# Performance work log

Hardware: AMD Instinct MI355X
Metric: run time of the kernel (lower is better)

## Reference

```python
import jax, jax.numpy as jnp
import numpy as np

HID = 2048   # hidden_size
H = 16       # num_attention_heads
KV = 2       # num_key_value_heads
HD = 256     # head_dim
S = 2048     # seq_len (prefill)
MAX_SEQ = 4096
EPS = 1e-6
RD = HD // 4          # partial RoPE dims (head_dim * 0.25)
SCALE = HD ** (-0.5)
GROUPS = H // KV


def setup_inputs() -> dict:
    key = jax.random.key(0)
    ks = jax.random.split(key, 10)
    hidden_in = jax.random.normal(ks[0], (1, S, HID), jnp.float32)
    ang = jax.random.uniform(ks[1], (1, S, RD), jnp.float32) * (2.0 * np.pi)
    cos = jnp.cos(ang)
    sin = jnp.sin(ang)
    w = 0.02
    q_proj_w = jax.random.normal(ks[2], (2 * H * HD, HID), jnp.float32) * w
    k_proj_w = jax.random.normal(ks[3], (KV * HD, HID), jnp.float32) * w
    v_proj_w = jax.random.normal(ks[4], (KV * HD, HID), jnp.float32) * w
    o_proj_w = jax.random.normal(ks[5], (HID, H * HD), jnp.float32) * w
    q_norm_w = jax.random.normal(ks[6], (HD,), jnp.float32) * 0.1
    k_norm_w = jax.random.normal(ks[7], (HD,), jnp.float32) * 0.1
    return dict(hidden_in=hidden_in, cos=cos, sin=sin,
                q_proj_w=q_proj_w, k_proj_w=k_proj_w, v_proj_w=v_proj_w,
                o_proj_w=o_proj_w, q_norm_w=q_norm_w, k_norm_w=k_norm_w)


def _rmsnorm(x, w):
    var = jnp.mean(x * x, axis=-1, keepdims=True)
    return x * jax.lax.rsqrt(var + EPS) * (1.0 + w)


def _rotate_half(x):
    x1, x2 = jnp.split(x, 2, axis=-1)
    return jnp.concatenate([-x2, x1], axis=-1)


def reference(hidden_in, cos, sin, q_proj_w, k_proj_w, v_proj_w, o_proj_w, q_norm_w, k_norm_w):
    # projections (F.linear => x @ W^T)
    qg = hidden_in @ q_proj_w.T                      # [1, S, 2*H*HD]
    k = hidden_in @ k_proj_w.T                       # [1, S, KV*HD]
    v = hidden_in @ v_proj_w.T

    qg = qg.reshape(1, S, H, 2 * HD)
    q, gate = qg[..., :HD], qg[..., HD:]             # chunk(2, dim=-1)
    gate = gate.reshape(1, S, H * HD)

    q = _rmsnorm(q, q_norm_w).transpose(0, 2, 1, 3)  # [1, H, S, HD]
    k = _rmsnorm(k.reshape(1, S, KV, HD), k_norm_w).transpose(0, 2, 1, 3)  # [1, KV, S, HD]
    v = v.reshape(1, S, KV, HD).transpose(0, 2, 1, 3)                      # [1, KV, S, HD]

    # partial RoPE on first RD dims
    c = cos[:, None, :, :]                           # [1, 1, S, RD]
    s = sin[:, None, :, :]
    q_rot, q_pass = q[..., :RD], q[..., RD:]
    k_rot, k_pass = k[..., :RD], k[..., RD:]
    q = jnp.concatenate([q_rot * c + _rotate_half(q_rot) * s, q_pass], axis=-1)
    k = jnp.concatenate([k_rot * c + _rotate_half(k_rot) * s, k_pass], axis=-1)

    # KV cache padded to max_seq
    zpad = jnp.zeros((1, KV, MAX_SEQ - S, HD), k.dtype)
    k_cache_out = jnp.concatenate([k, zpad], axis=2)
    v_cache_out = jnp.concatenate([v, zpad], axis=2)

    # GQA repeat
    k_r = jnp.repeat(k, GROUPS, axis=1)              # [1, H, S, HD]
    v_r = jnp.repeat(v, GROUPS, axis=1)

    causal = jnp.triu(jnp.full((S, S), -10000.0, jnp.float32), k=1)
    scores = jnp.einsum('bhqd,bhkd->bhqk', q, k_r) * SCALE + causal
    attn_w = jax.nn.softmax(scores, axis=-1)
    attn = jnp.einsum('bhqk,bhkd->bhqd', attn_w, v_r)
    attn = attn.transpose(0, 2, 1, 3).reshape(1, S, H * HD)

    attn = attn * jax.nn.sigmoid(gate)
    hidden_out = attn @ o_proj_w.T                   # [1, S, HID]
    return hidden_out, k_cache_out, v_cache_out
```

## Files before the change

### kernel.cpp

```cpp
#include <hip/hip_runtime.h>

#define S_LEN 2048
#define HID 2048
#define NH 16
#define NKV 2
#define HD 256
#define MAXSEQ 4096
#define NALL 9216
#define RD 64

typedef __attribute__((ext_vector_type(8))) short short8_t;
typedef __attribute__((ext_vector_type(4))) float float4_t;

#define DPPF(x, ctrl) __builtin_bit_cast(float, __builtin_amdgcn_update_dpp( \
    __builtin_bit_cast(int, x), __builtin_bit_cast(int, x), ctrl, 0xF, 0xF, false))

__device__ __forceinline__ unsigned short f2b(float f) {
  union { float f; unsigned u; } v; v.f = f;
  unsigned u = v.u;
  return (unsigned short)((u + 0x7FFFu + ((u >> 16) & 1u)) >> 16);
}

__device__ __forceinline__ void gload_lds16(const void* g, void* l) {
  __builtin_amdgcn_global_load_lds(
      (const __attribute__((address_space(1))) void*)g,
      (__attribute__((address_space(3))) void*)l, 16, 0, 0);
}

__global__ void fused_cvt(const float* __restrict__ hidden, const float* __restrict__ qw,
                          const float* __restrict__ kw, const float* __restrict__ vw,
                          const float* __restrict__ ow,
                          unsigned short* __restrict__ hidb, unsigned short* __restrict__ wallb,
                          unsigned short* __restrict__ wob,
                          float* __restrict__ kcache, float* __restrict__ vcache) {
  const long i = (long)blockIdx.x * 256 + threadIdx.x;
  const long N0 = 1048576, N1 = N0 + 4194304, N2 = N1 + 262144, N3 = N2 + 262144,
             N4 = N3 + 2097152;
  if (i < N4) {
    const float* s; unsigned short* d; long j;
    if (i < N0)      { s = hidden; d = hidb;  j = i; }
    else if (i < N1) { s = qw; d = wallb;                        j = i - N0; }
    else if (i < N2) { s = kw; d = wallb + (size_t)8192*HID;     j = i - N1; }
    else if (i < N3) { s = vw; d = wallb + (size_t)8704*HID;     j = i - N2; }
    else             { s = ow; d = wob;                          j = i - N3; }
    float4 v = ((const float4*)s)[j];
    short4 o;
    o.x = (short)f2b(v.x); o.y = (short)f2b(v.y);
    o.z = (short)f2b(v.z); o.w = (short)f2b(v.w);
    ((short4*)d)[j] = o;
  } else {
    long j = i - N4;
    int region = (int)(j >> 17);
    long o = j & 131071;
    float* base = (region < 2 ? kcache : vcache)
                + (size_t)(region & 1) * MAXSEQ * HD + (size_t)S_LEN * HD;
    float4 z; z.x = 0.f; z.y = 0.f; z.z = 0.f; z.w = 0.f;
    ((float4*)base)[o] = z;
  }
}

template<int BM, int BN, int MI, int NI>
__global__ __launch_bounds__(256, 2) void gemm_bt(
    const unsigned short* __restrict__ A, const unsigned short* __restrict__ B,
    float* __restrict__ C, int M, int N, int K) {
  constexpr int BK = 64;
  __shared__ unsigned short As[BM * BK];
  __shared__ unsigned short Bs[BN * BK];
  const int tid = threadIdx.x;
  const int lane = tid & 63;
  const int w = tid >> 6;
  const int wr = w >> 1, wc = w & 1;
  const int l15 = lane & 15, l4 = lane >> 4;
  const int M0 = blockIdx.y * BM, N0 = blockIdx.x * BN;
  float4_t acc[MI][NI] = {};
  for (int kt = 0; kt < K; kt += BK) {
    __syncthreads();
#pragma unroll
    for (int i = 0; i < BM/32; ++i) {
      int c = tid + i*256;
      int row = c >> 3;
      gload_lds16(A + (size_t)(M0 + row)*K + kt + ((c & 7) ^ (row & 7))*8, (char*)As + c*16);
    }
#pragma unroll
    for (int i = 0; i < BN/32; ++i) {
      int c = tid + i*256;
      int row = c >> 3;
      gload_lds16(B + (size_t)(N0 + row)*K + kt + ((c & 7) ^ (row & 7))*8, (char*)Bs + c*16);
    }
    __syncthreads();
#pragma unroll
    for (int ks = 0; ks < 2; ++ks) {
      short8_t af[MI], bf[NI];
#pragma unroll
      for (int mi = 0; mi < MI; ++mi) {
        int row = wr*(BM/2) + mi*16 + l15;
        af[mi] = *(const short8_t*)&As[row*BK + ((ks*4 + l4) ^ (l15 & 7))*8];
      }
#pragma unroll
      for (int ni = 0; ni < NI; ++ni) {
        int row = wc*(BN/2) + ni*16 + l15;
        bf[ni] = *(const short8_t*)&Bs[row*BK + ((ks*4 + l4) ^ (l15 & 7))*8];
      }
#pragma unroll
      for (int mi = 0; mi < MI; ++mi)
#pragma unroll
        for (int ni = 0; ni < NI; ++ni)
          acc[mi][ni] = __builtin_amdgcn_mfma_f32_16x16x32_bf16(af[mi], bf[ni], acc[mi][ni], 0, 0, 0);
    }
  }
#pragma unroll
  for (int mi = 0; mi < MI; ++mi) {
    int rb = M0 + wr*(BM/2) + mi*16 + l4*4;
#pragma unroll
    for (int ni = 0; ni < NI; ++ni) {
      int col = N0 + wc*(BN/2) + ni*16 + l15;
#pragma unroll
      for (int r = 0; r < 4; ++r)
        C[(size_t)(rb + r)*N + col] = acc[mi][ni][r];
    }
  }
}

__global__ void postproc(const float* __restrict__ C1,
                         const float* __restrict__ cosb, const float* __restrict__ sinb,
                         const float* __restrict__ qnw, const float* __restrict__ knw,
                         unsigned short* __restrict__ qb, unsigned short* __restrict__ kb,
                         unsigned short* __restrict__ vtb,
                         float* __restrict__ kcache, float* __restrict__ vcache) {
  const int w = threadIdx.x >> 6, lane = threadIdx.x & 63;
  const int s = blockIdx.x*4 + w;
  const int t = blockIdx.y;
  const int d = lane*4;
  const float* rowp;
  if (t < 16)      rowp = C1 + (size_t)s*NALL + t*512;
  else if (t < 18) rowp = C1 + (size_t)s*NALL + 8192 + (t-16)*256;
  else             rowp = C1 + (size_t)s*NALL + 8704 + (t-18)*256;
  float4 x = *(const float4*)(rowp + d);
  if (t >= 18) {
    int kvi = t - 18;
    *(float4*)(vcache + (size_t)kvi*MAXSEQ*HD + (size_t)s*HD + d) = x;
    unsigned short* vt = vtb + (size_t)kvi*HD*S_LEN;
    vt[(size_t)(d+0)*S_LEN + s] = f2b(x.x);
    vt[(size_t)(d+1)*S_LEN + s] = f2b(x.y);
    vt[(size_t)(d+2)*S_LEN + s] = f2b(x.z);
    vt[(size_t)(d+3)*S_LEN + s] = f2b(x.w);
    return;
  }
  float ss = x.x*x.x + x.y*x.y + x.z*x.z + x.w*x.w;
#pragma unroll
  for (int o = 32; o >= 1; o >>= 1) ss += __shfl_xor(ss, o, 64);
  float rn = rsqrtf(ss*(1.0f/256.0f) + 1e-6f);
  const float* nw = (t < 16) ? qnw : knw;
  float4 g = *(const float4*)(nw + d);
  float4 y;
  y.x = x.x*rn*(1.f+g.x); y.y = x.y*rn*(1.f+g.y);
  y.z = x.z*rn*(1.f+g.z); y.w = x.w*rn*(1.f+g.w);
  float px = __shfl_xor(y.x, 8, 64);
  float py = __shfl_xor(y.y, 8, 64);
  float pz = __shfl_xor(y.z, 8, 64);
  float pw = __shfl_xor(y.w, 8, 64);
  if (lane < 16) {
    float sgn = (lane & 8) ? 1.f : -1.f;
    float4 cs = *(const float4*)(cosb + (size_t)s*RD + d);
    float4 sn = *(const float4*)(sinb + (size_t)s*RD + d);
    y.x = y.x*cs.x + sgn*px*sn.x;
    y.y = y.y*cs.y + sgn*py*sn.y;
    y.z = y.z*cs.z + sgn*pz*sn.z;
    y.w = y.w*cs.w + sgn*pw*sn.w;
  }
  if (t < 16) {
    const float qs = 0.0625f * 1.44269504088896f;
    short4 o;
    o.x = (short)f2b(y.x*qs); o.y = (short)f2b(y.y*qs);
    o.z = (short)f2b(y.z*qs); o.w = (short)f2b(y.w*qs);
    *(short4*)(qb + (size_t)t*S_LEN*HD + (size_t)s*HD + d) = o;
  } else {
    int kvi = t - 16;
    *(float4*)(kcache + (size_t)kvi*MAXSEQ*HD + (size_t)s*HD + d) = y;
    short4 o;
    o.x = (short)f2b(y.x); o.y = (short)f2b(y.y);
    o.z = (short)f2b(y.z); o.w = (short)f2b(y.w);
    *(short4*)(kb + (size_t)kvi*S_LEN*HD + (size_t)s*HD + d) = o;
  }
}

__global__ __launch_bounds__(512, 2) void attn_kernel(
    const unsigned short* __restrict__ qb, const unsigned short* __restrict__ kb,
    const unsigned short* __restrict__ vtb, const float* __restrict__ C1,
    unsigned short* __restrict__ attnb) {
  __shared__ char smem[139264];
  const int tid = threadIdx.x, lane = tid & 63, w = tid >> 6;
  const int g  = w >> 2;
  const int wq = w & 3;
  const int l15 = lane & 15, l4 = lane >> 4;
  unsigned short* Pw = (unsigned short*)(smem + 131072 + w*1024);
  const int b = blockIdx.x;
  const int h = b & 15;
  const int pi = b >> 4;
  const int kv = h >> 3;
  const unsigned short* Qb = qb + (size_t)h*S_LEN*HD;
  const unsigned short* Kb = kb + (size_t)kv*S_LEN*HD;
  const unsigned short* Vb = vtb + (size_t)kv*HD*S_LEN;

  auto STAGE = [&](int k0s, int buf) {
    char* KsD = smem + buf*32768;
    char* VTD = smem + 65536 + buf*32768;
#pragma unroll
    for (int i = 0; i < 4; ++i) {
      int c = tid + i*512;
      int row = c >> 5;
      gload_lds16(Kb + (size_t)(k0s + row)*HD + ((c & 31) ^ (row & 7))*8, KsD + c*16);
    }
#pragma unroll
    for (int i = 0; i < 4; ++i) {
      int c = tid + i*512;
      int row = c >> 3;
      gload_lds16(Vb + (size_t)row*S_LEN + k0s + ((c & 7) ^ (row & 7))*8, VTD + c*16);
    }
  };

  for (int ph = 0; ph < 2; ++ph) {
    const int qt = ph ? (31 - pi) : pi;
    const int q0 = qt * 64;
    const int qrow = q0 + wq*16 + l15;
    short8_t qf[8];
#pragma unroll
    for (int kk = 0; kk < 8; ++kk)
      qf[kk] = *(const short8_t*)(Qb + (size_t)qrow*HD + kk*32 + l4*8);
    float4_t oacc[16] = {};
    float m_run[4] = {-1e29f, -1e29f, -1e29f, -1e29f};
    float l_run[4] = {0.f, 0.f, 0.f, 0.f};
    const int nT = qt + 1;
    __syncthreads();
    STAGE(0, 0);
    for (int t = 0; t < nT; ++t) {
      const int cur = t & 1;
      const int k0 = t * 64;
      if (t + 1 < nT) {
        STAGE((t + 1) * 64, cur ^ 1);
        asm volatile("s_waitcnt vmcnt(8)" ::: "memory");
      } else {
        asm volatile("s_waitcnt vmcnt(0)" ::: "memory");
      }
      __builtin_amdgcn_s_barrier();
      __builtin_amdgcn_sched_barrier(0);
      const unsigned short* Ks  = (const unsigned short*)(smem + cur*32768);
      const unsigned short* VTs = (const unsigned short*)(smem + 65536 + cur*32768);
      float4_t sacc[2] = {};
#pragma unroll
      for (int nt = 0; nt < 2; ++nt)
#pragma unroll
        for (int kk = 0; kk < 8; ++kk) {
          int krow = g*32 + nt*16 + l15;
          short8_t bfr = *(const short8_t*)&Ks[krow*HD + ((kk*4 + l4) ^ (l15 & 7))*8];
          sacc[nt] = __builtin_amdgcn_mfma_f32_16x16x32_bf16(qf[kk], bfr, sacc[nt], 0, 0, 0);
        }
      if (t == qt) {
#pragma unroll
        for (int nt = 0; nt < 2; ++nt)
#pragma unroll
          for (int r = 0; r < 4; ++r)
            if (k0 + g*32 + nt*16 + l15 > q0 + wq*16 + l4*4 + r) sacc[nt][r] = -1e30f;
      }
      float m0[4], p[2][4];
#pragma unroll
      for (int r = 0; r < 4; ++r) {
        float v = fmaxf(sacc[0][r], sacc[1][r]);
        v = fmaxf(v, DPPF(v, 0xB1));
        v = fmaxf(v, DPPF(v, 0x4E));
        v = fmaxf(v, DPPF(v, 0x141));
        v = fmaxf(v, DPPF(v, 0x140));
        m0[r] = v;
      }
      int need = (m0[0] > m_run[0] + 4.f) | (m0[1] > m_run[1] + 4.f) |
                 (m0[2] > m_run[2] + 4.f) | (m0[3] > m_run[3] + 4.f);
      if (__any(need)) {
        float al[4];
#pragma unroll
        for (int r = 0; r < 4; ++r) {
          float mnew = fmaxf(m_run[r], m0[r]);
          al[r] = exp2f(m_run[r] - mnew);
          m_run[r] = mnew;
          l_run[r] *= al[r];
        }
#pragma unroll
        for (int nt2 = 0; nt2 < 16; ++nt2) {
          oacc[nt2][0] *= al[0];
          oacc[nt2][1] *= al[1];
          oacc[nt2][2] *= al[2];
          oacc[nt2][3] *= al[3];
        }
      }
#pragma unroll
      for (int r = 0; r < 4; ++r) {
        p[0][r] = exp2f(sacc[0][r] - m_run[r]);
        p[1][r] = exp2f(sacc[1][r] - m_run[r]);
        float sum = p[0][r] + p[1][r];
        sum += DPPF(sum, 0xB1);
        sum += DPPF(sum, 0x4E);
        sum += DPPF(sum, 0x141);
        sum += DPPF(sum, 0x140);
        l_run[r] += sum;
      }
#pragma unroll
      for (int nt = 0; nt < 2; ++nt)
#pragma unroll
        for (int r = 0; r < 4; ++r) {
          int prow = l4*4 + r;
          int pcol = nt*16 + l15;
          Pw[prow*32 + (((pcol >> 3) ^ ((prow >> 1) & 3)))*8 + (pcol & 7)] = f2b(p[nt][r]);
        }
      short8_t pf = *(const short8_t*)&Pw[l15*32 + ((l4 ^ ((l15 >> 1) & 3)))*8];
#pragma unroll
      for (int nt2 = 0; nt2 < 16; ++nt2) {
        int vrow = nt2*16 + l15;
        short8_t v0 = *(const short8_t*)&VTs[vrow*64 + ((4*g + l4) ^ (vrow & 7))*8];
        oacc[nt2] = __builtin_amdgcn_mfma_f32_16x16x32_bf16(pf, v0, oacc[nt2], 0, 0, 0);
      }
      asm volatile("" ::: "memory");
      __builtin_amdgcn_s_barrier();
    }
    __syncthreads();
    float* Od = (float*)smem;
    float* ML = (float*)(smem + 69632);
    const int r0 = wq*16 + l4*4;
    if (g == 1) {
#pragma unroll
      for (int r = 0; r < 4; ++r)
        if (l15 == 0) { ML[(r0 + r)*2] = m_run[r]; ML[(r0 + r)*2 + 1] = l_run[r]; }
#pragma unroll
      for (int nt2 = 0; nt2 < 16; ++nt2) {
        int dim = nt2*16 + l15;
#pragma unroll
        for (int r = 0; r < 4; ++r)
          Od[(r0 + r)*258 + dim] = oacc[nt2][r];
      }
    }
    __syncthreads();
    if (g == 0) {
      float fA[4], fB[4], inv_l[4];
#pragma unroll
      for (int r = 0; r < 4; ++r) {
        float mB = ML[(r0 + r)*2];
        float lB = ML[(r0 + r)*2 + 1];
        float m = fmaxf(m_run[r], mB);
        fA[r] = exp2f(m_run[r] - m);
        fB[r] = exp2f(mB - m);
        inv_l[r] = 1.f / (l_run[r]*fA[r] + lB*fB[r]);
      }
      const int srow0 = q0 + r0;
#pragma unroll
      for (int nt2 = 0; nt2 < 16; ++nt2) {
        int dim = nt2*16 + l15;
#pragma unroll
        for (int r = 0; r < 4; ++r) {
          int srow = srow0 + r;
          float ov = oacc[nt2][r]*fA[r] + Od[(r0 + r)*258 + dim]*fB[r];
          float gv = C1[(size_t)srow*NALL + h*512 + 256 + dim];
          float sg = 1.f / (1.f + __expf(-gv));
          attnb[(size_t)srow*(NH*HD) + h*HD + dim] = f2b(ov * inv_l[r] * sg);
        }
      }
    }
  }
}

extern "C" void kernel_launch(void* const* d_in, const int* in_sizes, int n_in,
                              void* d_out, int out_size, void* d_ws, size_t ws_size,
                              hipStream_t stream) {
  const float* hidden = (const float*)d_in[0];
  const float* cosb   = (const float*)d_in[1];
  const float* sinb   = (const float*)d_in[2];
  const float* qw     = (const float*)d_in[3];
  const float* kw     = (const float*)d_in[4];
  const float* vw     = (const float*)d_in[5];
  const float* ow     = (const float*)d_in[6];
  const float* qnw    = (const float*)d_in[7];
  const float* knw    = (const float*)d_in[8];
  float* out    = (float*)d_out;
  float* kcache = out + (size_t)S_LEN*HID;
  float* vcache = kcache + (size_t)NKV*MAXSEQ*HD;

  char* ws = (char*)d_ws;
  size_t off = 0;
  auto alloc = [&](size_t bytes) -> char* {
    char* p = ws + off; off += (bytes + 255) & ~(size_t)255; return p;
  };
  unsigned short* hidb  = (unsigned short*)alloc((size_t)S_LEN*HID*2);
  unsigned short* wallb = (unsigned short*)alloc((size_t)NALL*HID*2);
  unsigned short* wob   = (unsigned short*)alloc((size_t)HID*NH*HD*2);
  float*          C1    = (float*)alloc((size_t)S_LEN*NALL*4);
  unsigned short* qb    = (unsigned short*)alloc((size_t)NH*S_LEN*HD*2);
  unsigned short* kb    = (unsigned short*)alloc((size_t)NKV*S_LEN*HD*2);
  unsigned short* vtb   = (unsigned short*)alloc((size_t)NKV*HD*S_LEN*2);
  unsigned short* attnb = (unsigned short*)alloc((size_t)S_LEN*NH*HD*2);

  fused_cvt<<<32768, 256, 0, stream>>>(hidden, qw, kw, vw, ow,
                                       hidb, wallb, wob, kcache, vcache);

  gemm_bt<128,128,4,4><<<dim3(NALL/128, S_LEN/128), 256, 0, stream>>>(
      hidb, wallb, C1, S_LEN, NALL, HID);

  postproc<<<dim3(S_LEN/4, 20), 256, 0, stream>>>(
      C1, cosb, sinb, qnw, knw, qb, kb, vtb, kcache, vcache);

  attn_kernel<<<256, 512, 0, stream>>>(qb, kb, vtb, C1, attnb);

  gemm_bt<128,64,4,2><<<dim3(HID/64, S_LEN/128), 256, 0, stream>>>(
      attnb, wob, out, S_LEN, HID, NH*HD);
}
```

Measured before the change: 405.9 us.

## Tile V transpose through LDS and prefetch V fragments with MFMA priority hints

Removes the scattered 2-byte strided V-transpose stores from postproc and adds a separate vt_transpose kernel that stages 64x64 tiles in LDS and writes coalesced short4 rows. In the attention inner loop, the V fragments are loaded from LDS right after the QK MFMAs, so the loads overlap the softmax work. The O rescale moves to just before the PV MFMAs, and s_setprio raises wave priority around the MFMA blocks. The cost is an extra kernel launch and higher register pressure from holding 16 V fragments per wave.

New measurement: 422.2 us. +4.0%, slower.

```diff
diff --git a/kernel.cpp b/kernel.cpp
--- a/kernel.cpp
+++ b/kernel.cpp
@@ -125,7 +125,6 @@
                          const float* __restrict__ cosb, const float* __restrict__ sinb,
                          const float* __restrict__ qnw, const float* __restrict__ knw,
                          unsigned short* __restrict__ qb, unsigned short* __restrict__ kb,
-                         unsigned short* __restrict__ vtb,
                          float* __restrict__ kcache, float* __restrict__ vcache) {
   const int w = threadIdx.x >> 6, lane = threadIdx.x & 63;
   const int s = blockIdx.x*4 + w;
@@ -139,11 +138,6 @@
   if (t >= 18) {
     int kvi = t - 18;
     *(float4*)(vcache + (size_t)kvi*MAXSEQ*HD + (size_t)s*HD + d) = x;
-    unsigned short* vt = vtb + (size_t)kvi*HD*S_LEN;
-    vt[(size_t)(d+0)*S_LEN + s] = f2b(x.x);
-    vt[(size_t)(d+1)*S_LEN + s] = f2b(x.y);
-    vt[(size_t)(d+2)*S_LEN + s] = f2b(x.z);
-    vt[(size_t)(d+3)*S_LEN + s] = f2b(x.w);
     return;
   }
   float ss = x.x*x.x + x.y*x.y + x.z*x.z + x.w*x.w;
@@ -184,6 +178,33 @@
   }
 }
 
+__global__ void vt_transpose(const float* __restrict__ C1,
+                             unsigned short* __restrict__ vtb) {
+  __shared__ unsigned short T[64][65];
+  const int b = blockIdx.x, i = threadIdx.x;
+  const int kvi = b >> 7, st = (b >> 2) & 31, dt = b & 3;
+  const int r = i >> 2;
+#pragma unroll
+  for (int jj = 0; jj < 4; ++jj) {
+    int c4 = (i & 3) + jj*4;
+    float4 x = *(const float4*)(C1 + (size_t)(st*64 + r)*NALL + 8704 + kvi*256
+                                + dt*64 + c4*4);
+    T[c4*4+0][r] = f2b(x.x);
+    T[c4*4+1][r] = f2b(x.y);
+    T[c4*4+2][r] = f2b(x.z);
+    T[c4*4+3][r] = f2b(x.w);
+  }
+  __syncthreads();
+  const int dr = i >> 2;
+  unsigned short* dst = vtb + (size_t)kvi*HD*S_LEN + (size_t)(dt*64 + dr)*S_LEN + st*64;
+#pragma unroll
+  for (int jj = 0; jj < 4; ++jj) {
+    int sc = (i & 3)*4 + jj*16;
+    short4 o = *(short4*)&T[dr][sc];
+    *(short4*)(dst + sc) = o;
+  }
+}
+
 __global__ __launch_bounds__(512, 2) void attn_kernel(
     const unsigned short* __restrict__ qb, const unsigned short* __restrict__ kb,
     const unsigned short* __restrict__ vtb, const float* __restrict__ C1,
@@ -247,6 +268,7 @@
       const unsigned short* Ks  = (const unsigned short*)(smem + cur*32768);
       const unsigned short* VTs = (const unsigned short*)(smem + 65536 + cur*32768);
       float4_t sacc[2] = {};
+      __builtin_amdgcn_s_setprio(1);
 #pragma unroll
       for (int nt = 0; nt < 2; ++nt)
 #pragma unroll
@@ -255,6 +277,13 @@
           short8_t bfr = *(const short8_t*)&Ks[krow*HD + ((kk*4 + l4) ^ (l15 & 7))*8];
           sacc[nt] = __builtin_amdgcn_mfma_f32_16x16x32_bf16(qf[kk], bfr, sacc[nt], 0, 0, 0);
         }
+      __builtin_amdgcn_s_setprio(0);
+      short8_t v0s[16];
+#pragma unroll
+      for (int nt2 = 0; nt2 < 16; ++nt2) {
+        int vrow = nt2*16 + l15;
+        v0s[nt2] = *(const short8_t*)&VTs[vrow*64 + ((4*g + l4) ^ (vrow & 7))*8];
+      }
       if (t == qt) {
 #pragma unroll
         for (int nt = 0; nt < 2; ++nt)
@@ -262,7 +291,7 @@
           for (int r = 0; r < 4; ++r)
             if (k0 + g*32 + nt*16 + l15 > q0 + wq*16 + l4*4 + r) sacc[nt][r] = -1e30f;
       }
-      float m0[4], p[2][4];
+      float m0[4], p[2][4], al[4];
 #pragma unroll
       for (int r = 0; r < 4; ++r) {
         float v = fmaxf(sacc[0][r], sacc[1][r]);
@@ -274,21 +303,14 @@
       }
       int need = (m0[0] > m_run[0] + 4.f) | (m0[1] > m_run[1] + 4.f) |
                  (m0[2] > m_run[2] + 4.f) | (m0[3] > m_run[3] + 4.f);
-      if (__any(need)) {
-        float al[4];
+      const int doresc = __any(need);
+      if (doresc) {
 #pragma unroll
         for (int r = 0; r < 4; ++r) {
           float mnew = fmaxf(m_run[r], m0[r]);
           al[r] = exp2f(m_run[r] - mnew);
           m_run[r] = mnew;
           l_run[r] *= al[r];
-        }
-#pragma unroll
-        for (int nt2 = 0; nt2 < 16; ++nt2) {
-          oacc[nt2][0] *= al[0];
-          oacc[nt2][1] *= al[1];
-          oacc[nt2][2] *= al[2];
-          oacc[nt2][3] *= al[3];
         }
       }
 #pragma unroll
@@ -311,12 +333,20 @@
           Pw[prow*32 + (((pcol >> 3) ^ ((prow >> 1) & 3)))*8 + (pcol & 7)] = f2b(p[nt][r]);
         }
       short8_t pf = *(const short8_t*)&Pw[l15*32 + ((l4 ^ ((l15 >> 1) & 3)))*8];
-#pragma unroll
-      for (int nt2 = 0; nt2 < 16; ++nt2) {
-        int vrow = nt2*16 + l15;
-        short8_t v0 = *(const short8_t*)&VTs[vrow*64 + ((4*g + l4) ^ (vrow & 7))*8];
-        oacc[nt2] = __builtin_amdgcn_mfma_f32_16x16x32_bf16(pf, v0, oacc[nt2], 0, 0, 0);
-      }
+      if (doresc) {
+#pragma unroll
+        for (int nt2 = 0; nt2 < 16; ++nt2) {
+          oacc[nt2][0] *= al[0];
+          oacc[nt2][1] *= al[1];
+          oacc[nt2][2] *= al[2];
+          oacc[nt2][3] *= al[3];
+        }
+      }
+      __builtin_amdgcn_s_setprio(1);
+#pragma unroll
+      for (int nt2 = 0; nt2 < 16; ++nt2)
+        oacc[nt2] = __builtin_amdgcn_mfma_f32_16x16x32_bf16(pf, v0s[nt2], oacc[nt2], 0, 0, 0);
+      __builtin_amdgcn_s_setprio(0);
       asm volatile("" ::: "memory");
       __builtin_amdgcn_s_barrier();
     }
@@ -402,7 +432,9 @@
       hidb, wallb, C1, S_LEN, NALL, HID);
 
   postproc<<<dim3(S_LEN/4, 20), 256, 0, stream>>>(
-      C1, cosb, sinb, qnw, knw, qb, kb, vtb, kcache, vcache);
+      C1, cosb, sinb, qnw, knw, qb, kb, kcache, vcache);
+
+  vt_transpose<<<256, 256, 0, stream>>>(C1, vtb);
 
   attn_kernel<<<256, 512, 0, stream>>>(qb, kb, vtb, C1, attnb);
 
```

## Double-buffer LDS tiles in bf16 GEMM to overlap global loads with MFMA

Applied to the files above, without the earlier changes.

The GEMM kernel now keeps two LDS buffers for the A and B tiles. It issues the async global-to-LDS loads for the next K tile before computing the current one, and uses explicit vmcnt waits and raw barriers in place of two __syncthreads per iteration. The goal is to hide global memory latency behind MFMA work. In exchange, LDS use per block doubles, which may reduce occupancy, and the hand-coded vmcnt counts depend on the per-thread load count matching the template configuration.

Result: slower. 423.9 us (+4.4%).

```diff
diff --git a/kernel.cpp b/kernel.cpp
--- a/kernel.cpp
+++ b/kernel.cpp
@@ -64,42 +64,60 @@
     const unsigned short* __restrict__ A, const unsigned short* __restrict__ B,
     float* __restrict__ C, int M, int N, int K) {
   constexpr int BK = 64;
-  __shared__ unsigned short As[BM * BK];
-  __shared__ unsigned short Bs[BN * BK];
+  constexpr int LOADS = BM/32 + BN/32;
+  __shared__ unsigned short As[2][BM * BK];
+  __shared__ unsigned short Bs[2][BN * BK];
   const int tid = threadIdx.x;
   const int lane = tid & 63;
   const int w = tid >> 6;
   const int wr = w >> 1, wc = w & 1;
   const int l15 = lane & 15, l4 = lane >> 4;
   const int M0 = blockIdx.y * BM, N0 = blockIdx.x * BN;
-  float4_t acc[MI][NI] = {};
-  for (int kt = 0; kt < K; kt += BK) {
-    __syncthreads();
+
+  auto STAGE = [&](int kt, int buf) {
 #pragma unroll
     for (int i = 0; i < BM/32; ++i) {
       int c = tid + i*256;
       int row = c >> 3;
-      gload_lds16(A + (size_t)(M0 + row)*K + kt + ((c & 7) ^ (row & 7))*8, (char*)As + c*16);
+      gload_lds16(A + (size_t)(M0 + row)*K + kt + ((c & 7) ^ (row & 7))*8,
+                  (char*)As[buf] + c*16);
     }
 #pragma unroll
     for (int i = 0; i < BN/32; ++i) {
       int c = tid + i*256;
       int row = c >> 3;
-      gload_lds16(B + (size_t)(N0 + row)*K + kt + ((c & 7) ^ (row & 7))*8, (char*)Bs + c*16);
-    }
-    __syncthreads();
+      gload_lds16(B + (size_t)(N0 + row)*K + kt + ((c & 7) ^ (row & 7))*8,
+                  (char*)Bs[buf] + c*16);
+    }
+  };
+
+  float4_t acc[MI][NI] = {};
+  const int nT = K / BK;
+  STAGE(0, 0);
+  for (int t = 0; t < nT; ++t) {
+    const int cur = t & 1;
+    if (t + 1 < nT) {
+      STAGE((t + 1) * BK, cur ^ 1);
+      if constexpr (LOADS == 8)      asm volatile("s_waitcnt vmcnt(8)" ::: "memory");
+      else if constexpr (LOADS == 6) asm volatile("s_waitcnt vmcnt(6)" ::: "memory");
+      else                           asm volatile("s_waitcnt vmcnt(0)" ::: "memory");
+    } else {
+      asm volatile("s_waitcnt vmcnt(0)" ::: "memory");
+    }
+    __builtin_amdgcn_s_barrier();
+    __builtin_amdgcn_sched_barrier(0);
 #pragma unroll
     for (int ks = 0; ks < 2; ++ks) {
       short8_t af[MI], bf[NI];
 #pragma unroll
       for (int mi = 0; mi < MI; ++mi) {
         int row = wr*(BM/2) + mi*16 + l15;
-        af[mi] = *(const short8_t*)&As[row*BK + ((ks*4 + l4) ^ (l15 & 7))*8];
+        af[mi] = *(const short8_t*)&As[cur][row*BK + ((ks*4 + l4) ^ (l15 & 7))*8];
       }
 #pragma unroll
       for (int ni = 0; ni < NI; ++ni) {
         int row = wc*(BN/2) + ni*16 + l15;
-        bf[ni] = *(const short8_t*)&Bs[row*BK + ((ks*4 + l4) ^ (l15 & 7))*8];
+        bf[ni] = *(const short8_t*)&Bs[cur][row*BK + ((ks*4 + l4) ^ (l15 & 7))*8];
       }
 #pragma unroll
       for (int mi = 0; mi < MI; ++mi)
@@ -107,6 +125,8 @@
         for (int ni = 0; ni < NI; ++ni)
           acc[mi][ni] = __builtin_amdgcn_mfma_f32_16x16x32_bf16(af[mi], bf[ni], acc[mi][ni], 0, 0, 0);
     }
+    asm volatile("" ::: "memory");
+    __builtin_amdgcn_s_barrier();
   }
 #pragma unroll
   for (int mi = 0; mi < MI; ++mi) {
```
